# Performance work log

Hardware: AMD Instinct MI355X
Metric: run time of the kernel (lower is better)

## Reference

```python
import jax, jax.numpy as jnp
import numpy as np

N_PTS = 1_000_000  # number of sample points (i index)
M_COMP = 64        # number of Gaussian components (j index)
D = 2


def setup_inputs() -> dict:
    key = jax.random.key(0)
    k1, k2, k3 = jax.random.split(key, 3)
    sample = jax.random.uniform(k1, (N_PTS, D), dtype=jnp.float32)
    mu = jax.random.uniform(k2, (M_COMP, D), dtype=jnp.float32)
    # Original init is A = 15 * I; add small noise so the Cholesky-like factor is generic.
    A = 15.0 * jnp.broadcast_to(jnp.eye(D, dtype=jnp.float32), (M_COMP, D, D)) \
        + 0.5 * jax.random.normal(k3, (M_COMP, D, D), dtype=jnp.float32)
    w = jnp.ones((M_COMP, 1), dtype=jnp.float32)
    return {"sample": sample, "mu": mu, "A": A, "w": w}


def reference(sample, mu, A, w):
    """log_likelihoods(sample): log sum_j weights_j * exp(-(x_i-mu_j)^T G_j (x_i-mu_j))."""
    M = A.shape[0]
    # gamma_j = A_j A_j^T / 2  (symmetric, M x D x D)
    gamma = jnp.einsum('jkm,jlm->jkl', A, A) / 2
    g = gamma.reshape(M, D * D)  # (M, 4), row-major [g00, g01, g10, g11]
    # batched 2x2 determinant (covariances_determinants)
    dets = g[:, 0] * g[:, 3] - g[:, 1] * g[:, 2]  # (M,)
    # weights_log = log_softmax(w) + 0.5 * log(det)
    wlog = jax.nn.log_softmax(w, axis=0)[:, 0] + 0.5 * jnp.log(dets)  # (M,)
    # Weighted squared distance q_ij = (x_i - mu_j)^T G_j (x_i - mu_j),
    # expanded to avoid the (N, M, D) difference tensor:
    xx = jnp.stack([sample[:, 0] * sample[:, 0],
                    sample[:, 0] * sample[:, 1],
                    sample[:, 1] * sample[:, 0],
                    sample[:, 1] * sample[:, 1]], axis=1)  # (N, 4)
    quad_x = xx @ g.T                                      # (N, M)
    Gmu = jnp.einsum('jkl,jl->jk', gamma, mu)              # (M, D)
    cross = sample @ Gmu.T                                 # (N, M)
    const = jnp.einsum('jk,jk->j', mu, Gmu)                # (M,)
    K = -(quad_x - 2.0 * cross + const[None, :])           # (N, M) log-kernel
    # weighted logsumexp over components j
    ll = jax.nn.logsumexp(K + wlog[None, :], axis=1, keepdims=True)  # (N, 1)
    return ll
```

## Files before the change

### kernel.cpp

```cpp
#include <hip/hip_runtime.h>
#include <math.h>

#define N_PTS  1000000
#define M_COMP 64

typedef float v2f __attribute__((ext_vector_type(2)));

__device__ __forceinline__ float exp2n(float x) { return __builtin_amdgcn_exp2f(x); }
__device__ __forceinline__ float log2n(float x) { return __builtin_amdgcn_logf(x); }

__global__ __launch_bounds__(256) void gm_fused(
    const float* __restrict__ sample,
    const float* __restrict__ mu,
    const float* __restrict__ A,
    const float* __restrict__ w,
    float* __restrict__ out)
{
    __shared__ float cf[6 * M_COMP];

    const int tid = threadIdx.x;
    const float L2E = 1.4426950408889634f;
    const float LN2 = 0.6931471805599453f;

    if (tid < 64) {
        const int j = tid;
        const float a00 = A[j*4+0], a01 = A[j*4+1], a10 = A[j*4+2], a11 = A[j*4+3];
        const float g00 = 0.5f*(a00*a00 + a01*a01);
        const float g01 = 0.5f*(a00*a10 + a01*a11);
        const float g11 = 0.5f*(a10*a10 + a11*a11);
        const float det = g00*g11 - g01*g01;

        const float m0 = mu[j*2+0], m1 = mu[j*2+1];
        const float Gmu0 = g00*m0 + g01*m1;
        const float Gmu1 = g01*m0 + g11*m1;
        const float cst  = m0*Gmu0 + m1*Gmu1;

        const float wj = w[j];
        float mx = wj;
        #pragma unroll
        for (int m = 1; m < 64; m <<= 1)
            mx = fmaxf(mx, __shfl_xor(mx, m, 64));
        float se = exp2n((wj - mx) * L2E);
        #pragma unroll
        for (int m = 1; m < 64; m <<= 1)
            se += __shfl_xor(se, m, 64);
        const float lse  = mx + log2n(se) * LN2;
        const float wlog = wj - lse + 0.5f * log2n(det) * LN2;

        cf[0*M_COMP+j] = -g00 * L2E;
        cf[1*M_COMP+j] = -(g01+g01) * L2E;
        cf[2*M_COMP+j] = -g11 * L2E;
        cf[3*M_COMP+j] = (Gmu0+Gmu0) * L2E;
        cf[4*M_COMP+j] = (Gmu1+Gmu1) * L2E;
        cf[5*M_COMP+j] = (wlog - cst) * L2E;
    }
    __syncthreads();

    const int t  = blockIdx.x * 256 + tid;
    const int p0 = t * 2;
    const bool ok = p0 < N_PTS;
    const int  pl = ok ? p0 : 0;

    const float4 q = ((const float4*)sample)[pl >> 1];

    const float x0v[2]  = {q.x, q.z};
    const float x1v[2]  = {q.y, q.w};
    float xx0v[2], x01v[2], xx1v[2];
    #pragma unroll
    for (int p = 0; p < 2; ++p) {
        xx0v[p] = x0v[p]*x0v[p];
        x01v[p] = x0v[p]*x1v[p];
        xx1v[p] = x1v[p]*x1v[p];
    }

    v2f acc[2] = {{0.f,0.f},{0.f,0.f}};

    #pragma unroll 2
    for (int jc = 0; jc < M_COMP; jc += 4) {
        const float4 c0 = *(const float4*)&cf[0*M_COMP+jc];
        const float4 c1 = *(const float4*)&cf[1*M_COMP+jc];
        const float4 c2 = *(const float4*)&cf[2*M_COMP+jc];
        const float4 c3 = *(const float4*)&cf[3*M_COMP+jc];
        const float4 c4 = *(const float4*)&cf[4*M_COMP+jc];
        const float4 c5 = *(const float4*)&cf[5*M_COMP+jc];

        const v2f c0lo = {c0.x, c0.y}, c0hi = {c0.z, c0.w};
        const v2f c1lo = {c1.x, c1.y}, c1hi = {c1.z, c1.w};
        const v2f c2lo = {c2.x, c2.y}, c2hi = {c2.z, c2.w};
        const v2f c3lo = {c3.x, c3.y}, c3hi = {c3.z, c3.w};
        const v2f c4lo = {c4.x, c4.y}, c4hi = {c4.z, c4.w};
        const v2f c5lo = {c5.x, c5.y}, c5hi = {c5.z, c5.w};

        #pragma unroll
        for (int p = 0; p < 2; ++p) {
            const v2f X0  = {x0v[p],  x0v[p]};
            const v2f X1  = {x1v[p],  x1v[p]};
            const v2f XX0 = {xx0v[p], xx0v[p]};
            const v2f X01 = {x01v[p], x01v[p]};
            const v2f XX1 = {xx1v[p], xx1v[p]};

            v2f s = c5lo;
            s = __builtin_elementwise_fma(c4lo, X1,  s);
            s = __builtin_elementwise_fma(c3lo, X0,  s);
            s = __builtin_elementwise_fma(c2lo, XX1, s);
            s = __builtin_elementwise_fma(c1lo, X01, s);
            s = __builtin_elementwise_fma(c0lo, XX0, s);
            acc[p][0] += exp2n(s[0]);
            acc[p][1] += exp2n(s[1]);

            v2f r = c5hi;
            r = __builtin_elementwise_fma(c4hi, X1,  r);
            r = __builtin_elementwise_fma(c3hi, X0,  r);
            r = __builtin_elementwise_fma(c2hi, XX1, r);
            r = __builtin_elementwise_fma(c1hi, X01, r);
            r = __builtin_elementwise_fma(c0hi, XX0, r);
            acc[p][0] += exp2n(r[0]);
            acc[p][1] += exp2n(r[1]);
        }
    }

    if (ok) {
        float2 o;
        o.x = log2n(acc[0][0] + acc[0][1]) * LN2;
        o.y = log2n(acc[1][0] + acc[1][1]) * LN2;
        *(float2*)&out[p0] = o;
    }
}

extern "C" void kernel_launch(void* const* d_in, const int* in_sizes, int n_in,
                              void* d_out, int out_size, void* d_ws, size_t ws_size,
                              hipStream_t stream)
{
    const float* sample = (const float*)d_in[0];
    const float* mu     = (const float*)d_in[1];
    const float* A      = (const float*)d_in[2];
    const float* w      = (const float*)d_in[3];
    float* out = (float*)d_out;

    const int blocks = (N_PTS/2 + 255) / 256;
    gm_fused<<<blocks, 256, 0, stream>>>(sample, mu, A, w, out);
}
```

Baseline: 17.54 us.

## Compute Gaussian log-kernel via bf16 MFMA with hi/lo split and persistent waves

Replaces the per-thread FMA evaluation of the quadratic form with 16x16x32 bf16 MFMA calls. Coefficients and point features are split into high and low bf16 parts so that cross products recover near-fp32 accuracy. The launch becomes a persistent grid of 977 blocks, where each wave loops over 16-point tiles and reduces the exp2 sums with lane shuffles. The aim is to move the FMA work onto matrix cores, leaving the exp2 calls as the main VALU cost. The costs are bf16 rounding risk, since the lo*lo term is dropped, and lower per-thread parallelism.

```diff
diff --git a/kernel.cpp b/kernel.cpp
--- a/kernel.cpp
+++ b/kernel.cpp
@@ -3,13 +3,30 @@
 
 #define N_PTS  1000000
 #define M_COMP 64
+#define TILES  (N_PTS / 16)
+#define NBLK   977
+#define NWAVES (NBLK * 4)
 
-typedef float v2f __attribute__((ext_vector_type(2)));
+typedef float        f32x4  __attribute__((ext_vector_type(4)));
+typedef short        bf16x8 __attribute__((ext_vector_type(8)));
+typedef unsigned int u32;
+typedef u32          u32x4  __attribute__((ext_vector_type(4)));
 
-__device__ __forceinline__ float exp2n(float x) { return __builtin_amdgcn_exp2f(x); }
-__device__ __forceinline__ float log2n(float x) { return __builtin_amdgcn_logf(x); }
+__device__ __forceinline__ float exp2n(float x){ return __builtin_amdgcn_exp2f(x); }
+__device__ __forceinline__ float log2n(float x){ return __builtin_amdgcn_logf(x); }
+__device__ __forceinline__ u32   fbits(float x){ return __builtin_bit_cast(u32, x); }
+__device__ __forceinline__ float trunch(float x){
+    return __builtin_bit_cast(float, fbits(x) & 0xffff0000u);
+}
+__device__ __forceinline__ u32 pk(float a, float b){
+    return (fbits(a) >> 16) | (fbits(b) & 0xffff0000u);
+}
+__device__ __forceinline__ bf16x8 frag(u32 a, u32 b, u32 c){
+    u32x4 t = {a, b, c, 0u};
+    return __builtin_bit_cast(bf16x8, t);
+}
 
-__global__ __launch_bounds__(256) void gm_fused(
+__global__ __launch_bounds__(256) void gm_mfma(
     const float* __restrict__ sample,
     const float* __restrict__ mu,
     const float* __restrict__ A,
@@ -56,74 +73,69 @@
     }
     __syncthreads();
 
-    const int t  = blockIdx.x * 256 + tid;
-    const int p0 = t * 2;
-    const bool ok = p0 < N_PTS;
-    const int  pl = ok ? p0 : 0;
+    const int lane = tid & 63;
+    const int col  = lane & 15;
+    const int kg   = lane >> 4;
+    const int wid  = (blockIdx.x * 256 + tid) >> 6;
 
-    const float4 q = ((const float4*)sample)[pl >> 1];
+    const bool gLo = (kg == 2);
+    const bool gZr = (kg == 3);
+    bf16x8 Ag0, Ag1, Ag2, Ag3;
+#define MKA(T, DST) {                                                        \
+        const int c = col + 16*(T);                                          \
+        const float g0 = cf[0*M_COMP+c], g1 = cf[1*M_COMP+c];                \
+        const float g2 = cf[2*M_COMP+c], g3 = cf[3*M_COMP+c];                \
+        const float g4 = cf[4*M_COMP+c], g5 = cf[5*M_COMP+c];                \
+        const u32 GH0 = pk(g0,g1), GH1 = pk(g2,g3), GH2 = pk(g4,g5);         \
+        const float e0 = g0-trunch(g0), e1 = g1-trunch(g1);                  \
+        const float e2 = g2-trunch(g2), e3 = g3-trunch(g3);                  \
+        const float e4 = g4-trunch(g4), e5 = g5-trunch(g5);                  \
+        const u32 GL0 = pk(e0,e1), GL1 = pk(e2,e3), GL2 = pk(e4,e5);         \
+        const u32 a0 = gZr ? 0u : (gLo ? GL0 : GH0);                         \
+        const u32 a1 = gZr ? 0u : (gLo ? GL1 : GH1);                         \
+        const u32 a2 = gZr ? 0u : (gLo ? GL2 : GH2);                         \
+        DST = frag(a0, a1, a2); }
+    MKA(0, Ag0) MKA(1, Ag1) MKA(2, Ag2) MKA(3, Ag3)
+#undef MKA
 
-    const float x0v[2]  = {q.x, q.z};
-    const float x1v[2]  = {q.y, q.w};
-    float xx0v[2], x01v[2], xx1v[2];
-    #pragma unroll
-    for (int p = 0; p < 2; ++p) {
-        xx0v[p] = x0v[p]*x0v[p];
-        x01v[p] = x0v[p]*x1v[p];
-        xx1v[p] = x1v[p]*x1v[p];
-    }
+    const bool bLo = (kg == 1);
+    const bool bZr = (kg == 3);
+    const f32x4 zero = {0.f, 0.f, 0.f, 0.f};
+    const float2* s2 = (const float2*)sample;
 
-    v2f acc[2] = {{0.f,0.f},{0.f,0.f}};
+    #pragma unroll 1
+    for (int i = 0; i < 16; ++i) {
+        const int tt = wid + NWAVES * i;
+        if (tt >= TILES) break;
+        const int pbase = tt * 16;
 
-    #pragma unroll 2
-    for (int jc = 0; jc < M_COMP; jc += 4) {
-        const float4 c0 = *(const float4*)&cf[0*M_COMP+jc];
-        const float4 c1 = *(const float4*)&cf[1*M_COMP+jc];
-        const float4 c2 = *(const float4*)&cf[2*M_COMP+jc];
-        const float4 c3 = *(const float4*)&cf[3*M_COMP+jc];
-        const float4 c4 = *(const float4*)&cf[4*M_COMP+jc];
-        const float4 c5 = *(const float4*)&cf[5*M_COMP+jc];
+        const float2 xy = s2[pbase + col];
+        const float x0 = xy.x, x1 = xy.y;
+        const float f0 = x0*x0, f1 = x0*x1, f2 = x1*x1;
+        const float l0 = f0 - trunch(f0), l1 = f1 - trunch(f1);
+        const float l2 = f2 - trunch(f2);
+        const float l3 = x0 - trunch(x0), l4 = x1 - trunch(x1);
+        const u32 H0 = pk(f0, f1), H1 = pk(f2, x0), H2 = pk(x1, 1.0f);
+        const u32 L0 = pk(l0, l1), L1 = pk(l2, l3), L2 = pk(l4, 0.0f);
+        const u32 b0 = bZr ? 0u : (bLo ? L0 : H0);
+        const u32 b1 = bZr ? 0u : (bLo ? L1 : H1);
+        const u32 b2 = bZr ? 0u : (bLo ? L2 : H2);
+        const bf16x8 Bf = frag(b0, b1, b2);
 
-        const v2f c0lo = {c0.x, c0.y}, c0hi = {c0.z, c0.w};
-        const v2f c1lo = {c1.x, c1.y}, c1hi = {c1.z, c1.w};
-        const v2f c2lo = {c2.x, c2.y}, c2hi = {c2.z, c2.w};
-        const v2f c3lo = {c3.x, c3.y}, c3hi = {c3.z, c3.w};
-        const v2f c4lo = {c4.x, c4.y}, c4hi = {c4.z, c4.w};
-        const v2f c5lo = {c5.x, c5.y}, c5hi = {c5.z, c5.w};
+        f32x4 c0 = __builtin_amdgcn_mfma_f32_16x16x32_bf16(Ag0, Bf, zero, 0, 0, 0);
+        f32x4 c1 = __builtin_amdgcn_mfma_f32_16x16x32_bf16(Ag1, Bf, zero, 0, 0, 0);
+        f32x4 c2 = __builtin_amdgcn_mfma_f32_16x16x32_bf16(Ag2, Bf, zero, 0, 0, 0);
+        f32x4 c3 = __builtin_amdgcn_mfma_f32_16x16x32_bf16(Ag3, Bf, zero, 0, 0, 0);
 
+        float sum = 0.f;
         #pragma unroll
-        for (int p = 0; p < 2; ++p) {
-            const v2f X0  = {x0v[p],  x0v[p]};
-            const v2f X1  = {x1v[p],  x1v[p]};
-            const v2f XX0 = {xx0v[p], xx0v[p]};
-            const v2f X01 = {x01v[p], x01v[p]};
-            const v2f XX1 = {xx1v[p], xx1v[p]};
+        for (int r = 0; r < 4; ++r)
+            sum += exp2n(c0[r]) + exp2n(c1[r]) + exp2n(c2[r]) + exp2n(c3[r]);
+        sum += __shfl_xor(sum, 16, 64);
+        sum += __shfl_xor(sum, 32, 64);
 
-            v2f s = c5lo;
-            s = __builtin_elementwise_fma(c4lo, X1,  s);
-            s = __builtin_elementwise_fma(c3lo, X0,  s);
-            s = __builtin_elementwise_fma(c2lo, XX1, s);
-            s = __builtin_elementwise_fma(c1lo, X01, s);
-            s = __builtin_elementwise_fma(c0lo, XX0, s);
-            acc[p][0] += exp2n(s[0]);
-            acc[p][1] += exp2n(s[1]);
-
-            v2f r = c5hi;
-            r = __builtin_elementwise_fma(c4hi, X1,  r);
-            r = __builtin_elementwise_fma(c3hi, X0,  r);
-            r = __builtin_elementwise_fma(c2hi, XX1, r);
-            r = __builtin_elementwise_fma(c1hi, X01, r);
-            r = __builtin_elementwise_fma(c0hi, XX0, r);
-            acc[p][0] += exp2n(r[0]);
-            acc[p][1] += exp2n(r[1]);
-        }
-    }
-
-    if (ok) {
-        float2 o;
-        o.x = log2n(acc[0][0] + acc[0][1]) * LN2;
-        o.y = log2n(acc[1][0] + acc[1][1]) * LN2;
-        *(float2*)&out[p0] = o;
+        if (lane < 16)
+            out[pbase + lane] = log2n(sum) * LN2;
     }
 }
 
@@ -137,6 +149,5 @@
     const float* w      = (const float*)d_in[3];
     float* out = (float*)d_out;
 
-    const int blocks = (N_PTS/2 + 255) / 256;
-    gm_fused<<<blocks, 256, 0, stream>>>(sample, mu, A, w, out);
+    gm_mfma<<<NBLK, 256, 0, stream>>>(sample, mu, A, w, out);
 }
```

After: 24.57 us. 40.1% more time.
